# Performance work log

Measured on AMD Instinct MI355X. Metric: run time of the kernel, lower is better.

The kernel has to match this reference:

```python
import jax, jax.numpy as jnp
import numpy as np

INPUT_SIZE = 512
HIDDEN_SIZE = 1024
OUTPUT_SIZE = 10
BATCH = 64
SEQ_LEN = 512


def _linear_init(key, out_f, in_f):
    # torch nn.Linear default init: U(-1/sqrt(in_f), 1/sqrt(in_f))
    kw, kb = jax.random.split(key)
    bound = 1.0 / np.sqrt(in_f)
    w = jax.random.uniform(kw, (out_f, in_f), jnp.float32, -bound, bound)
    b = jax.random.uniform(kb, (out_f,), jnp.float32, -bound, bound)
    return w, b


def setup_inputs() -> dict:
    key = jax.random.key(0)
    ks = jax.random.split(key, 6)
    comb = INPUT_SIZE + HIDDEN_SIZE
    Wf_w, Wf_b = _linear_init(ks[0], HIDDEN_SIZE, comb)
    Wi_w, Wi_b = _linear_init(ks[1], HIDDEN_SIZE, comb)
    Wo_w, Wo_b = _linear_init(ks[2], HIDDEN_SIZE, comb)
    Wc_w, Wc_b = _linear_init(ks[3], HIDDEN_SIZE, comb)
    out_w, out_b = _linear_init(ks[4], OUTPUT_SIZE, HIDDEN_SIZE)
    input_seq = jax.random.normal(ks[5], (BATCH, SEQ_LEN, INPUT_SIZE), jnp.float32)
    return {
        "input_seq": input_seq,
        "Wf_w": Wf_w, "Wf_b": Wf_b,
        "Wi_w": Wi_w, "Wi_b": Wi_b,
        "Wo_w": Wo_w, "Wo_b": Wo_b,
        "Wc_w": Wc_w, "Wc_b": Wc_b,
        "out_w": out_w, "out_b": out_b,
    }


def reference(input_seq, Wf_w, Wf_b, Wi_w, Wi_b, Wo_w, Wo_b, Wc_w, Wc_b, out_w, out_b):
    B, S, I = input_seq.shape
    H = Wf_w.shape[0]
    # Fuse the 4 gate GEMMs into one [I+H, 4H] matmul per step (same math).
    W = jnp.concatenate([Wf_w, Wi_w, Wo_w, Wc_w], axis=0).T  # [I+H, 4H]
    b = jnp.concatenate([Wf_b, Wi_b, Wo_b, Wc_b])             # [4H]

    def step(carry, x_t):
        h, c = carry                               # [B,H], [B,H]
        comb = jnp.concatenate([x_t, h], axis=1)   # [B, I+H]
        gates = comb @ W + b                       # [B, 4H]
        f, i, o, g = jnp.split(gates, 4, axis=1)
        c_new = jax.nn.sigmoid(f) * c + jax.nn.sigmoid(i) * jnp.tanh(g)
        h_new = jax.nn.sigmoid(o) * jnp.tanh(c_new)
        return (h_new, c_new), None

    h0 = jnp.zeros((B, H), input_seq.dtype)
    c0 = jnp.zeros((B, H), input_seq.dtype)
    (h_T, _), _ = jax.lax.scan(step, (h0, c0), input_seq.transpose(1, 0, 2))
    logits = h_T @ out_w.T + out_b  # [B, output_size]
    return logits
```

## Files before the change

### kernel.cpp

```cpp
#include <hip/hip_runtime.h>


typedef _Float16 f16;
typedef _Float16 f16x8 __attribute__((ext_vector_type(8)));
typedef float f32x4 __attribute__((ext_vector_type(4)));
typedef unsigned short u16;
typedef unsigned int u32;

#define NBLK 128
#define SEQ 512

#define XH_OFF 0ull
#define XH_BYTES (64ull * 512 * 512 * 2)
#define WPRE_OFF (XH_OFF + XH_BYTES)
#define WPRE_BYTES (128ull * 48 * 2 * 64 * 16)
#define BIAS_OFF (WPRE_OFF + WPRE_BYTES)
#define BIAS_BYTES (128ull * 32 * 4)
#define HBUF_OFF (BIAS_OFF + BIAS_BYTES)
#define HBUF_BYTES (2ull * 32 * 64 * 4 * 16)
#define HFIN_OFF (HBUF_OFF + HBUF_BYTES)
#define HFIN_BYTES (64ull * 1024 * 4)
#define FLG_OFF (HFIN_OFF + HFIN_BYTES)
#define FLG_BYTES (512ull * 128 * 4)
#define WS_NEEDED (FLG_OFF + FLG_BYTES)

__global__ void prep_kernel(const float* __restrict__ xin,
                            const float* __restrict__ wf, const float* __restrict__ wi,
                            const float* __restrict__ wo, const float* __restrict__ wc,
                            const float* __restrict__ bfp, const float* __restrict__ bip,
                            const float* __restrict__ bop, const float* __restrict__ bcp,
                            f16* __restrict__ x_h, f16x8* __restrict__ W_pre,
                            float* __restrict__ bias_pre, u32* __restrict__ flagz,
                            u32* __restrict__ hzero) {
  long long id = (long long)blockIdx.x * 256 + threadIdx.x;
  const long long NX = 16777216;
  const long long NW = 786432;
  const long long NB_ = 4096;
  const long long NF = 65536;
  const long long NH = 32768;
  if (id < NX) {
    int b = (int)(id >> 18);
    int t = (int)((id >> 9) & 511);
    int k = (int)(id & 511);
    x_h[(((long long)t * 64 + b) << 9) | k] = (f16)xin[id];
  } else if ((id -= NX) < NW) {
    int lane = (int)(id & 63);
    int nt = (int)((id >> 6) & 1);
    int ktbl = (int)(id >> 7);
    int kt = ktbl % 48;
    int bl = ktbl / 48;
    int c = nt * 16 + (lane & 15);
    int g = c >> 3;
    int j = bl * 8 + (c & 7);
    int kbase = kt * 32 + 8 * (lane >> 4);
    const float* src = (g == 0) ? wf : (g == 1) ? wi : (g == 2) ? wo : wc;
    const float* row = src + (long long)j * 1536 + kbase;
    f16x8 v;
#pragma unroll
    for (int e = 0; e < 8; ++e) v[e] = (f16)row[e];
    W_pre[id] = v;
  } else if ((id -= NW) < NB_) {
    int bl = (int)(id >> 5);
    int c = (int)(id & 31);
    int g = c >> 3;
    int j = bl * 8 + (c & 7);
    const float* src = (g == 0) ? bfp : (g == 1) ? bip : (g == 2) ? bop : bcp;
    bias_pre[id] = src[j];
  } else if ((id -= NB_) < NF) {
    flagz[id] = 0u;
  } else if ((id -= NF) < NH) {
    hzero[id] = 0u;
  }
}

__device__ __forceinline__ float sgm(float x) { return 1.0f / (1.0f + __expf(-x)); }
__device__ __forceinline__ float tnh(float x) { return 1.0f - 2.0f / (__expf(2.0f * x) + 1.0f); }

__device__ __forceinline__ void ld16_sc1(f16x8* dst, const f16x8* p) {
  asm volatile("global_load_dwordx4 %0, %1, off sc1" : "=v"(*dst) : "v"(p) : "memory");
}
__device__ __forceinline__ void st16_sc1(f16x8* p, f16x8 v) {
  asm volatile("global_store_dwordx4 %0, %1, off sc1" : : "v"(p), "v"(v) : "memory");
}

__global__ __launch_bounds__(256, 1) void lstm_kernel(const f16* __restrict__ x_h,
                                                      const f16x8* __restrict__ W_pre,
                                                      const float* __restrict__ bias_pre,
                                                      f16x8* hfrag, float* hfinal, u32* flag) {
  __shared__ f16x8 Wlds[48 * 2 * 64];
  __shared__ f16 hstage[64 * 8];
  const int tid = threadIdx.x;
  const int bl = blockIdx.x;
  const int lane = tid & 63;
  const int wv = tid >> 6;

  {
    const f16x8* src = W_pre + (long long)bl * (48 * 2 * 64);
    for (int i = tid; i < 48 * 2 * 64; i += 256) Wlds[i] = src[i];
  }
  __syncthreads();

  const int l15 = lane & 15;
  const int lq = lane >> 4;
  const int arow = 16 * wv + l15;
  const float bias0 = bias_pre[bl * 32 + l15];
  const float bias1 = bias_pre[bl * 32 + 16 + l15];
  const int jcol = bl * 8 + (lane & 7);
  const bool act = (l15 < 8);
  const int wkt = bl >> 2;
  const int wlq = bl & 3;
  float cst0 = 0.f, cst1 = 0.f, cst2 = 0.f, cst3 = 0.f;

  f32x4 xacc[2][2];

  auto xgemm = [&](int T) {
    f32x4 z = {0.f, 0.f, 0.f, 0.f};
    xacc[0][0] = z; xacc[0][1] = z; xacc[1][0] = z; xacc[1][1] = z;
    const f16* xr = x_h + (((long long)T * 64 + arow) << 9) + 8 * lq;
    f16x8 xf[16];
#pragma unroll
    for (int kk = 0; kk < 16; ++kk) xf[kk] = *(const f16x8*)(xr + kk * 32);
#pragma unroll
    for (int kk = 0; kk < 16; ++kk) {
      f16x8 b0 = Wlds[(kk * 2 + 0) * 64 + lane];
      f16x8 b1 = Wlds[(kk * 2 + 1) * 64 + lane];
      xacc[0][kk & 1] = __builtin_amdgcn_mfma_f32_16x16x32_f16(xf[kk], b0, xacc[0][kk & 1], 0, 0, 0);
      xacc[1][kk & 1] = __builtin_amdgcn_mfma_f32_16x16x32_f16(xf[kk], b1, xacc[1][kk & 1], 0, 0, 0);
    }
  };

  xgemm(0);

  for (int t = 0; t < SEQ; ++t) {
    const f16x8* hb = hfrag + (size_t)(t & 1) * 8192;
    f16x8* hwv_buf = hfrag + (size_t)((t + 1) & 1) * 8192;

    f32x4 acc00 = xacc[0][0], acc01 = xacc[0][1];
    f32x4 acc10 = xacc[1][0], acc11 = xacc[1][1];

    const f16x8* hb0 = hb + arow * 4 + lq;
    f16x8 hfr[32];
#pragma unroll
    for (int kt = 0; kt < 32; ++kt) ld16_sc1(&hfr[kt], hb0 + kt * 256);
    asm volatile("s_waitcnt vmcnt(0)" ::: "memory");
    __builtin_amdgcn_sched_barrier(0);
#pragma unroll
    for (int kt = 0; kt < 32; ++kt) {
      f16x8 b0 = Wlds[((16 + kt) * 2 + 0) * 64 + lane];
      f16x8 b1 = Wlds[((16 + kt) * 2 + 1) * 64 + lane];
      if (kt & 1) {
        acc01 = __builtin_amdgcn_mfma_f32_16x16x32_f16(hfr[kt], b0, acc01, 0, 0, 0);
        acc11 = __builtin_amdgcn_mfma_f32_16x16x32_f16(hfr[kt], b1, acc11, 0, 0, 0);
      } else {
        acc00 = __builtin_amdgcn_mfma_f32_16x16x32_f16(hfr[kt], b0, acc00, 0, 0, 0);
        acc10 = __builtin_amdgcn_mfma_f32_16x16x32_f16(hfr[kt], b1, acc10, 0, 0, 0);
      }
    }

    f32x4 g0 = acc00 + acc01;
    f32x4 g1 = acc10 + acc11;
#pragma unroll
    for (int r = 0; r < 4; ++r) { g0[r] += bias0; g1[r] += bias1; }

    float iv0 = __shfl_xor(g0[0], 8), iv1 = __shfl_xor(g0[1], 8);
    float iv2 = __shfl_xor(g0[2], 8), iv3 = __shfl_xor(g0[3], 8);
    float gv0 = __shfl_xor(g1[0], 8), gv1 = __shfl_xor(g1[1], 8);
    float gv2 = __shfl_xor(g1[2], 8), gv3 = __shfl_xor(g1[3], 8);

    if (act) {
      const int brb = 16 * wv + 4 * lq;
#pragma unroll
      for (int r = 0; r < 4; ++r) {
        float fpre = (r == 0) ? g0[0] : (r == 1) ? g0[1] : (r == 2) ? g0[2] : g0[3];
        float opre = (r == 0) ? g1[0] : (r == 1) ? g1[1] : (r == 2) ? g1[2] : g1[3];
        float ipre = (r == 0) ? iv0 : (r == 1) ? iv1 : (r == 2) ? iv2 : iv3;
        float gpre = (r == 0) ? gv0 : (r == 1) ? gv1 : (r == 2) ? gv2 : gv3;
        float cold = (r == 0) ? cst0 : (r == 1) ? cst1 : (r == 2) ? cst2 : cst3;
        float cn = sgm(fpre) * cold + sgm(ipre) * tnh(gpre);
        float hv = sgm(opre) * tnh(cn);
        if (r == 0) cst0 = cn; else if (r == 1) cst1 = cn; else if (r == 2) cst2 = cn; else cst3 = cn;
        int row = brb + r;
        hstage[row * 8 + l15] = (f16)hv;
        if (t == SEQ - 1) hfinal[row * 1024 + jcol] = hv;
      }
    }

    __syncthreads();
    if (tid < 64) {
      f16x8 hrow = *(const f16x8*)&hstage[tid * 8];
      st16_sc1(hwv_buf + (wkt * 256 + tid * 4 + wlq), hrow);
    }

    __syncthreads();
    if (t + 1 < SEQ) {
      if (tid == 0)
        __hip_atomic_store(&flag[(size_t)t * NBLK + bl], 1u, __ATOMIC_RELAXED,
                           __HIP_MEMORY_SCOPE_AGENT);
      xgemm(t + 1);
      if (wv == 0) {
        const u32* fl = flag + (size_t)t * NBLK;
        u32 it = 0;
        while (true) {
          u32 a = __hip_atomic_load(fl + 2 * lane, __ATOMIC_RELAXED, __HIP_MEMORY_SCOPE_AGENT);
          u32 b = __hip_atomic_load(fl + 2 * lane + 1, __ATOMIC_RELAXED, __HIP_MEMORY_SCOPE_AGENT);
          if (__all((a & b) == 1u)) break;
          __builtin_amdgcn_s_sleep(1);
          if (++it > 50000u) break;
        }
      }
      __syncthreads();
    }
  }
}

__global__ void logits_kernel(const float* __restrict__ hfinal, const float* __restrict__ ow,
                              const float* __restrict__ ob, float* __restrict__ out) {
  int b = blockIdx.x / 10;
  int o = blockIdx.x % 10;
  int lane = threadIdx.x;
  const float* hrow = hfinal + b * 1024;
  const float* wrow = ow + o * 1024;
  float s = 0.f;
#pragma unroll 4
  for (int i = lane; i < 1024; i += 64) s += hrow[i] * wrow[i];
#pragma unroll
  for (int off = 32; off; off >>= 1) s += __shfl_xor(s, off);
  if (lane == 0) out[b * 10 + o] = s + ob[o];
}

extern "C" void kernel_launch(void* const* d_in, const int* in_sizes, int n_in,
                              void* d_out, int out_size, void* d_ws, size_t ws_size,
                              hipStream_t stream) {
  const float* xin = (const float*)d_in[0];
  const float* wf = (const float*)d_in[1];
  const float* bf = (const float*)d_in[2];
  const float* wi = (const float*)d_in[3];
  const float* bi = (const float*)d_in[4];
  const float* wo = (const float*)d_in[5];
  const float* bo = (const float*)d_in[6];
  const float* wc = (const float*)d_in[7];
  const float* bc = (const float*)d_in[8];
  const float* ow = (const float*)d_in[9];
  const float* ob = (const float*)d_in[10];
  (void)in_sizes; (void)n_in; (void)out_size;

  if (ws_size < WS_NEEDED) return;
  char* ws = (char*)d_ws;
  f16* x_h = (f16*)(ws + XH_OFF);
  f16x8* W_pre = (f16x8*)(ws + WPRE_OFF);
  float* bias_pre = (float*)(ws + BIAS_OFF);
  f16x8* hfrag = (f16x8*)(ws + HBUF_OFF);
  float* hfinal = (float*)(ws + HFIN_OFF);
  u32* flag = (u32*)(ws + FLG_OFF);

  const long long total = 16777216LL + 786432 + 4096 + 65536 + 32768;
  const int pblocks = (int)((total + 255) / 256);
  prep_kernel<<<pblocks, 256, 0, stream>>>(xin, wf, wi, wo, wc, bf, bi, bo, bc, x_h, W_pre,
                                           bias_pre, flag, (u32*)hfrag);
  lstm_kernel<<<NBLK, 256, 0, stream>>>(x_h, W_pre, bias_pre, hfrag, hfinal, flag);
  logits_kernel<<<640, 64, 0, stream>>>(hfinal, ow, ob, (float*)d_out);
}
```

Baseline: 4.025 ms.

## Split K dimension across two wave groups per block with LDS reduction

```diff
diff --git a/kernel.cpp b/kernel.cpp
--- a/kernel.cpp
+++ b/kernel.cpp
@@ -83,26 +83,29 @@
   asm volatile("global_store_dwordx4 %0, %1, off sc1" : : "v"(p), "v"(v) : "memory");
 }
 
-__global__ __launch_bounds__(256, 1) void lstm_kernel(const f16* __restrict__ x_h,
+__global__ __launch_bounds__(512, 1) void lstm_kernel(const f16* __restrict__ x_h,
                                                       const f16x8* __restrict__ W_pre,
                                                       const float* __restrict__ bias_pre,
                                                       f16x8* hfrag, float* hfinal, u32* flag) {
   __shared__ f16x8 Wlds[48 * 2 * 64];
+  __shared__ f32x4 comb[4 * 64 * 2];
   __shared__ f16 hstage[64 * 8];
   const int tid = threadIdx.x;
   const int bl = blockIdx.x;
   const int lane = tid & 63;
   const int wv = tid >> 6;
+  const int grp = wv >> 2;
+  const int mwv = wv & 3;
 
   {
     const f16x8* src = W_pre + (long long)bl * (48 * 2 * 64);
-    for (int i = tid; i < 48 * 2 * 64; i += 256) Wlds[i] = src[i];
+    for (int i = tid; i < 48 * 2 * 64; i += 512) Wlds[i] = src[i];
   }
   __syncthreads();
 
   const int l15 = lane & 15;
   const int lq = lane >> 4;
-  const int arow = 16 * wv + l15;
+  const int arow = 16 * mwv + l15;
   const float bias0 = bias_pre[bl * 32 + l15];
   const float bias1 = bias_pre[bl * 32 + 16 + l15];
   const int jcol = bl * 8 + (lane & 7);
@@ -117,15 +120,16 @@
     f32x4 z = {0.f, 0.f, 0.f, 0.f};
     xacc[0][0] = z; xacc[0][1] = z; xacc[1][0] = z; xacc[1][1] = z;
     const f16* xr = x_h + (((long long)T * 64 + arow) << 9) + 8 * lq;
-    f16x8 xf[16];
-#pragma unroll
-    for (int kk = 0; kk < 16; ++kk) xf[kk] = *(const f16x8*)(xr + kk * 32);
-#pragma unroll
-    for (int kk = 0; kk < 16; ++kk) {
+    f16x8 xf[8];
+#pragma unroll
+    for (int j = 0; j < 8; ++j) xf[j] = *(const f16x8*)(xr + (2 * j + grp) * 32);
+#pragma unroll
+    for (int j = 0; j < 8; ++j) {
+      int kk = 2 * j + grp;
       f16x8 b0 = Wlds[(kk * 2 + 0) * 64 + lane];
       f16x8 b1 = Wlds[(kk * 2 + 1) * 64 + lane];
-      xacc[0][kk & 1] = __builtin_amdgcn_mfma_f32_16x16x32_f16(xf[kk], b0, xacc[0][kk & 1], 0, 0, 0);
-      xacc[1][kk & 1] = __builtin_amdgcn_mfma_f32_16x16x32_f16(xf[kk], b1, xacc[1][kk & 1], 0, 0, 0);
+      xacc[0][j & 1] = __builtin_amdgcn_mfma_f32_16x16x32_f16(xf[j], b0, xacc[0][j & 1], 0, 0, 0);
+      xacc[1][j & 1] = __builtin_amdgcn_mfma_f32_16x16x32_f16(xf[j], b1, xacc[1][j & 1], 0, 0, 0);
     }
   };
 
@@ -139,63 +143,73 @@
     f32x4 acc10 = xacc[1][0], acc11 = xacc[1][1];
 
     const f16x8* hb0 = hb + arow * 4 + lq;
-    f16x8 hfr[32];
-#pragma unroll
-    for (int kt = 0; kt < 32; ++kt) ld16_sc1(&hfr[kt], hb0 + kt * 256);
+    f16x8 hfr[16];
+#pragma unroll
+    for (int j = 0; j < 16; ++j) ld16_sc1(&hfr[j], hb0 + (2 * j + grp) * 256);
     asm volatile("s_waitcnt vmcnt(0)" ::: "memory");
     __builtin_amdgcn_sched_barrier(0);
 #pragma unroll
-    for (int kt = 0; kt < 32; ++kt) {
+    for (int j = 0; j < 16; ++j) {
+      int kt = 2 * j + grp;
       f16x8 b0 = Wlds[((16 + kt) * 2 + 0) * 64 + lane];
       f16x8 b1 = Wlds[((16 + kt) * 2 + 1) * 64 + lane];
-      if (kt & 1) {
-        acc01 = __builtin_amdgcn_mfma_f32_16x16x32_f16(hfr[kt], b0, acc01, 0, 0, 0);
-        acc11 = __builtin_amdgcn_mfma_f32_16x16x32_f16(hfr[kt], b1, acc11, 0, 0, 0);
+      if (j & 1) {
+        acc01 = __builtin_amdgcn_mfma_f32_16x16x32_f16(hfr[j], b0, acc01, 0, 0, 0);
+        acc11 = __builtin_amdgcn_mfma_f32_16x16x32_f16(hfr[j], b1, acc11, 0, 0, 0);
       } else {
-        acc00 = __builtin_amdgcn_mfma_f32_16x16x32_f16(hfr[kt], b0, acc00, 0, 0, 0);
-        acc10 = __builtin_amdgcn_mfma_f32_16x16x32_f16(hfr[kt], b1, acc10, 0, 0, 0);
-      }
-    }
-
-    f32x4 g0 = acc00 + acc01;
-    f32x4 g1 = acc10 + acc11;
-#pragma unroll
-    for (int r = 0; r < 4; ++r) { g0[r] += bias0; g1[r] += bias1; }
-
-    float iv0 = __shfl_xor(g0[0], 8), iv1 = __shfl_xor(g0[1], 8);
-    float iv2 = __shfl_xor(g0[2], 8), iv3 = __shfl_xor(g0[3], 8);
-    float gv0 = __shfl_xor(g1[0], 8), gv1 = __shfl_xor(g1[1], 8);
-    float gv2 = __shfl_xor(g1[2], 8), gv3 = __shfl_xor(g1[3], 8);
-
-    if (act) {
-      const int brb = 16 * wv + 4 * lq;
-#pragma unroll
-      for (int r = 0; r < 4; ++r) {
-        float fpre = (r == 0) ? g0[0] : (r == 1) ? g0[1] : (r == 2) ? g0[2] : g0[3];
-        float opre = (r == 0) ? g1[0] : (r == 1) ? g1[1] : (r == 2) ? g1[2] : g1[3];
-        float ipre = (r == 0) ? iv0 : (r == 1) ? iv1 : (r == 2) ? iv2 : iv3;
-        float gpre = (r == 0) ? gv0 : (r == 1) ? gv1 : (r == 2) ? gv2 : gv3;
-        float cold = (r == 0) ? cst0 : (r == 1) ? cst1 : (r == 2) ? cst2 : cst3;
-        float cn = sgm(fpre) * cold + sgm(ipre) * tnh(gpre);
-        float hv = sgm(opre) * tnh(cn);
-        if (r == 0) cst0 = cn; else if (r == 1) cst1 = cn; else if (r == 2) cst2 = cn; else cst3 = cn;
-        int row = brb + r;
-        hstage[row * 8 + l15] = (f16)hv;
-        if (t == SEQ - 1) hfinal[row * 1024 + jcol] = hv;
-      }
-    }
-
+        acc00 = __builtin_amdgcn_mfma_f32_16x16x32_f16(hfr[j], b0, acc00, 0, 0, 0);
+        acc10 = __builtin_amdgcn_mfma_f32_16x16x32_f16(hfr[j], b1, acc10, 0, 0, 0);
+      }
+    }
+
+    f32x4 p0 = acc00 + acc01;
+    f32x4 p1 = acc10 + acc11;
+    if (grp == 1) {
+      comb[(mwv * 64 + lane) * 2 + 0] = p0;
+      comb[(mwv * 64 + lane) * 2 + 1] = p1;
+    }
     __syncthreads();
-    if (tid < 64) {
-      f16x8 hrow = *(const f16x8*)&hstage[tid * 8];
-      st16_sc1(hwv_buf + (wkt * 256 + tid * 4 + wlq), hrow);
+
+    if (grp == 0) {
+      f32x4 g0 = p0 + comb[(mwv * 64 + lane) * 2 + 0];
+      f32x4 g1 = p1 + comb[(mwv * 64 + lane) * 2 + 1];
+#pragma unroll
+      for (int r = 0; r < 4; ++r) { g0[r] += bias0; g1[r] += bias1; }
+
+      float iv0 = __shfl_xor(g0[0], 8), iv1 = __shfl_xor(g0[1], 8);
+      float iv2 = __shfl_xor(g0[2], 8), iv3 = __shfl_xor(g0[3], 8);
+      float gv0 = __shfl_xor(g1[0], 8), gv1 = __shfl_xor(g1[1], 8);
+      float gv2 = __shfl_xor(g1[2], 8), gv3 = __shfl_xor(g1[3], 8);
+
+      if (act) {
+        const int brb = 16 * mwv + 4 * lq;
+#pragma unroll
+        for (int r = 0; r < 4; ++r) {
+          float fpre = (r == 0) ? g0[0] : (r == 1) ? g0[1] : (r == 2) ? g0[2] : g0[3];
+          float opre = (r == 0) ? g1[0] : (r == 1) ? g1[1] : (r == 2) ? g1[2] : g1[3];
+          float ipre = (r == 0) ? iv0 : (r == 1) ? iv1 : (r == 2) ? iv2 : iv3;
+          float gpre = (r == 0) ? gv0 : (r == 1) ? gv1 : (r == 2) ? gv2 : gv3;
+          float cold = (r == 0) ? cst0 : (r == 1) ? cst1 : (r == 2) ? cst2 : cst3;
+          float cn = sgm(fpre) * cold + sgm(ipre) * tnh(gpre);
+          float hv = sgm(opre) * tnh(cn);
+          if (r == 0) cst0 = cn; else if (r == 1) cst1 = cn; else if (r == 2) cst2 = cn; else cst3 = cn;
+          int row = brb + r;
+          hstage[row * 8 + l15] = (f16)hv;
+          if (t == SEQ - 1) hfinal[row * 1024 + jcol] = hv;
+        }
+      }
     }
 
     __syncthreads();
     if (t + 1 < SEQ) {
-      if (tid == 0)
-        __hip_atomic_store(&flag[(size_t)t * NBLK + bl], 1u, __ATOMIC_RELAXED,
-                           __HIP_MEMORY_SCOPE_AGENT);
+      if (tid < 64) {
+        f16x8 hrow = *(const f16x8*)&hstage[tid * 8];
+        st16_sc1(hwv_buf + (wkt * 256 + tid * 4 + wlq), hrow);
+        asm volatile("s_waitcnt vmcnt(0)" ::: "memory");
+        if (tid == 0)
+          __hip_atomic_store(&flag[(size_t)t * NBLK + bl], 1u, __ATOMIC_RELAXED,
+                             __HIP_MEMORY_SCOPE_AGENT);
+      }
       xgemm(t + 1);
       if (wv == 0) {
         const u32* fl = flag + (size_t)t * NBLK;
@@ -257,6 +271,6 @@
   const int pblocks = (int)((total + 255) / 256);
   prep_kernel<<<pblocks, 256, 0, stream>>>(xin, wf, wi, wo, wc, bf, bi, bo, bc, x_h, W_pre,
                                            bias_pre, flag, (u32*)hfrag);
-  lstm_kernel<<<NBLK, 256, 0, stream>>>(x_h, W_pre, bias_pre, hfrag, hfinal, flag);
+  lstm_kernel<<<NBLK, 512, 0, stream>>>(x_h, W_pre, bias_pre, hfrag, hfinal, flag);
   logits_kernel<<<640, 64, 0, stream>>>(hfinal, ow, ob, (float*)d_out);
 }
```

Result: faster. 3.294 ms (-18.2%).
